# Performance work log

Hardware: AMD Instinct MI355X
Metric: run time of the kernel (lower is better)

The kernel has to match this reference:

```python
import jax, jax.numpy as jnp
import numpy as np

EPS = 1e-06


def setup_inputs() -> dict:
    key = jax.random.key(0)
    ks = jax.random.split(key, 6)
    B, H, S, W = 1, 12, 768, 32
    attn_logits = jax.random.normal(ks[0], (B, H, S, S), dtype=jnp.float32)
    # shared first linear: Linear(1, mlp_width) -> weight [W,1], bias [W]
    W_in = jax.random.normal(ks[1], (W, 1), dtype=jnp.float32) * (1.0)
    b_in = jax.random.normal(ks[2], (W,), dtype=jnp.float32) * 0.1
    # per-head output linear: Linear(mlp_width, 1) -> weight [H, W], bias [H]
    W_out = jax.random.normal(ks[3], (H, W), dtype=jnp.float32) / np.sqrt(W)
    b_out = jax.random.normal(ks[4], (H,), dtype=jnp.float32) * 0.1
    c = jnp.asarray(0.1, dtype=jnp.float32)
    L_multiplier = jnp.asarray(1.0, dtype=jnp.float32)
    init_L = jnp.asarray(512.0, dtype=jnp.float32)  # requires_grad=False in torch
    return {"attn_logits": attn_logits, "W_in": W_in, "b_in": b_in,
            "W_out": W_out, "b_out": b_out, "c": c,
            "L_multiplier": L_multiplier, "init_L": init_L}


def reference(attn_logits, W_in, b_in, W_out, b_out, c, L_multiplier, init_L):
    # gates and reverse cumulative sum along the key axis
    gates = jax.nn.sigmoid(attn_logits)                      # [B,H,S,S]
    pos = jax.lax.cumsum(gates, axis=3, reverse=True)        # flip-cumsum-flip
    numerator = jnp.log(jnp.abs(c * pos) + 1.0)
    max_pos = pos[..., 0:1]                                  # [B,H,S,1]
    threshold = jnp.abs(L_multiplier * init_L)
    denominator = jnp.log(jnp.abs(c * jnp.minimum(max_pos, threshold)) + 1.0) + EPS
    dist = numerator / denominator                           # [B,H,S,S]
    # shared Linear(1,W) + ReLU, then per-head Linear(W,1)
    w1 = W_in[:, 0]                                          # [W]
    hidden = jax.nn.relu(dist[..., None] * w1 + b_in)        # [B,H,S,S,W]
    fire_bias = jnp.einsum('bhijw,hw->bhij', hidden, W_out) + b_out[None, :, None, None]
    return fire_bias
```

## Files before the change

### kernel.cpp

```cpp
#include <hip/hip_runtime.h>

#define EPS_F 1e-6f
#define S_DIM 768
#define W_DIM 32

__global__ __launch_bounds__(256) void cope_fire_kernel(
    const float* __restrict__ attn,
    const float* __restrict__ W_in,
    const float* __restrict__ b_in,
    const float* __restrict__ W_out,
    const float* __restrict__ b_out,
    const float* __restrict__ c_p,
    const float* __restrict__ Lm_p,
    const float* __restrict__ iL_p,
    float* __restrict__ out)
{
    const int row = blockIdx.x;
    const int h   = row / S_DIM;
    const int t   = threadIdx.x;
    const int lane = t & 63;
    const int wave = t >> 6;

    __shared__ float s_w1[W_DIM], s_bin[W_DIM], s_wout[W_DIM];
    __shared__ float s_wsum[12];

    if (t < W_DIM) {
        s_w1[t]   = W_in[t];
        s_bin[t]  = b_in[t];
        s_wout[t] = W_out[h * W_DIM + t];
    }

    const float* rowp = attn + (size_t)row * S_DIM;
    const float c   = c_p[0];
    const float thr = fabsf(Lm_p[0] * iL_p[0]);
    const float bo  = b_out[h];

    float g[3];
#pragma unroll
    for (int s = 0; s < 3; s++) {
        float x = rowp[s * 256 + t];
        g[s] = 1.0f / (1.0f + expf(-x));
    }

    float incl[3];
#pragma unroll
    for (int s = 0; s < 3; s++) {
        float x = g[s];
#pragma unroll
        for (int d = 1; d < 64; d <<= 1) {
            float y = __shfl_up(x, d, 64);
            if (lane >= d) x += y;
        }
        if (lane == 63) s_wsum[s * 4 + wave] = x;
        incl[s] = x;
    }
    __syncthreads();

    float segtot[3];
#pragma unroll
    for (int s = 0; s < 3; s++) {
        float w0 = s_wsum[s * 4 + 0];
        float w1 = s_wsum[s * 4 + 1];
        float w2 = s_wsum[s * 4 + 2];
        float w3 = s_wsum[s * 4 + 3];
        float woff = 0.0f;
        if (wave > 0) woff += w0;
        if (wave > 1) woff += w1;
        if (wave > 2) woff += w2;
        incl[s] += woff;
        segtot[s] = w0 + w1 + w2 + w3;
    }
    const float off1  = segtot[0];
    const float off2  = segtot[0] + segtot[1];
    const float total = off2 + segtot[2];
    incl[1] += off1;
    incl[2] += off2;

    const float den = logf(fabsf(c * fminf(total, thr)) + 1.0f) + EPS_F;
    const float inv_den = 1.0f / den;

    float* outp = out + (size_t)row * S_DIM;
#pragma unroll
    for (int s = 0; s < 3; s++) {
        float pos  = total - incl[s] + g[s];
        float dist = logf(fabsf(c * pos) + 1.0f) * inv_den;
        float acc = bo;
#pragma unroll
        for (int w = 0; w < W_DIM; w++) {
            float hv = fmaxf(dist * s_w1[w] + s_bin[w], 0.0f);
            acc += hv * s_wout[w];
        }
        outp[s * 256 + t] = acc;
    }
}

extern "C" void kernel_launch(void* const* d_in, const int* in_sizes, int n_in,
                              void* d_out, int out_size, void* d_ws, size_t ws_size,
                              hipStream_t stream) {
    const float* attn  = (const float*)d_in[0];
    const float* W_in  = (const float*)d_in[1];
    const float* b_in  = (const float*)d_in[2];
    const float* W_out = (const float*)d_in[3];
    const float* b_out = (const float*)d_in[4];
    const float* c_p   = (const float*)d_in[5];
    const float* Lm_p  = (const float*)d_in[6];
    const float* iL_p  = (const float*)d_in[7];
    float* out = (float*)d_out;

    const int H = 12;
    const int rows = H * S_DIM;
    cope_fire_kernel<<<rows, 256, 0, stream>>>(
        attn, W_in, b_in, W_out, b_out, c_p, Lm_p, iL_p, out);
}
```

Baseline: 126.5 us.

## Replace per-element MLP with piecewise-linear lookup over sorted ReLU breakpoints

A setup kernel sorts the ReLU breakpoints -b/w of the shared first linear layer and precomputes per-head slope/intercept pairs for each of the 33 intervals. The main kernel then computes each output as one FMA after a binary search over the breakpoints, instead of a 32-wide hidden-layer loop. It also maps one row per wavefront with 12 contiguous elements per lane, float4 loads and stores, a single wave-level scan, and fast exp/log/rcp intrinsics. The cost is an extra tiny kernel launch and small float rounding differences from the reassociated arithmetic and fast math.

```diff
diff --git a/kernel.cpp b/kernel.cpp
--- a/kernel.cpp
+++ b/kernel.cpp
@@ -1,97 +1,135 @@
 #include <hip/hip_runtime.h>
+#include <math.h>
 
 #define EPS_F 1e-6f
 #define S_DIM 768
 #define W_DIM 32
+#define H_DIM 12
+#define NK 33
+
+
+__global__ __launch_bounds__(512) void cope_setup_kernel(
+    const float* __restrict__ W_in, const float* __restrict__ b_in,
+    const float* __restrict__ W_out, const float* __restrict__ b_out,
+    float* __restrict__ ws)
+{
+    __shared__ float th[W_DIM];
+    __shared__ int   rk[W_DIM];
+    const int t = threadIdx.x;
+
+    if (t < W_DIM) {
+        float w1 = W_in[t], b = b_in[t];
+        th[t] = (w1 != 0.0f) ? (-b / w1) : __builtin_inff();
+    }
+    __syncthreads();
+
+    if (t < W_DIM) {
+        float mine = th[t];
+        int r = 0;
+        for (int v = 0; v < W_DIM; v++) {
+            float o = th[v];
+            if (o < mine || (o == mine && v < t)) r++;
+        }
+        rk[t] = r;
+        ws[r] = mine;
+    }
+    __syncthreads();
+
+    if (t < H_DIM * NK) {
+        int h = t / NK, k = t % NK;
+        float A = 0.0f, B = b_out[h];
+        for (int w = 0; w < W_DIM; w++) {
+            float w1 = W_in[w], bv = b_in[w], ov = W_out[h * W_DIM + w];
+            bool active = (w1 > 0.0f) ? (k > rk[w])
+                        : (w1 < 0.0f) ? (k <= rk[w])
+                        : (bv > 0.0f);
+            if (active) { A += w1 * ov; B += bv * ov; }
+        }
+        ws[W_DIM + h * 2 * NK + 2 * k]     = A;
+        ws[W_DIM + h * 2 * NK + 2 * k + 1] = B;
+    }
+}
 
 __global__ __launch_bounds__(256) void cope_fire_kernel(
     const float* __restrict__ attn,
-    const float* __restrict__ W_in,
-    const float* __restrict__ b_in,
-    const float* __restrict__ W_out,
-    const float* __restrict__ b_out,
     const float* __restrict__ c_p,
     const float* __restrict__ Lm_p,
     const float* __restrict__ iL_p,
+    const float* __restrict__ ws,
     float* __restrict__ out)
 {
-    const int row = blockIdx.x;
-    const int h   = row / S_DIM;
-    const int t   = threadIdx.x;
+    const int t    = threadIdx.x;
     const int lane = t & 63;
     const int wave = t >> 6;
+    const int row  = blockIdx.x * 4 + wave;
+    const int h    = blockIdx.x / (S_DIM / 4);
 
-    __shared__ float s_w1[W_DIM], s_bin[W_DIM], s_wout[W_DIM];
-    __shared__ float s_wsum[12];
+    __shared__ float sh[W_DIM];
+    __shared__ float sAB[2 * NK];
 
-    if (t < W_DIM) {
-        s_w1[t]   = W_in[t];
-        s_bin[t]  = b_in[t];
-        s_wout[t] = W_out[h * W_DIM + t];
+    if (t < W_DIM)  sh[t]  = ws[t];
+    if (t < 2 * NK) sAB[t] = ws[W_DIM + h * 2 * NK + t];
+
+    const float s3 = ws[3],  s7 = ws[7],  s11 = ws[11], s15 = ws[15];
+    const float s19 = ws[19], s23 = ws[23], s27 = ws[27];
+    const float c   = c_p[0];
+    const float thr = fabsf(Lm_p[0] * iL_p[0]);
+
+    const float* rowp = attn + (size_t)row * S_DIM + lane * 12;
+    float4 v0 = *(const float4*)(rowp);
+    float4 v1 = *(const float4*)(rowp + 4);
+    float4 v2 = *(const float4*)(rowp + 8);
+    float g[12] = { v0.x, v0.y, v0.z, v0.w, v1.x, v1.y, v1.z, v1.w,
+                    v2.x, v2.y, v2.z, v2.w };
+#pragma unroll
+    for (int i = 0; i < 12; i++)
+        g[i] = __builtin_amdgcn_rcpf(1.0f + __expf(-g[i]));
+
+    float T0 = 0.0f;
+#pragma unroll
+    for (int i = 0; i < 12; i++) T0 += g[i];
+    float P = T0;
+#pragma unroll
+    for (int d = 1; d < 64; d <<= 1) {
+        float y = __shfl_up(P, d, 64);
+        if (lane >= d) P += y;
+    }
+    const float total = __shfl(P, 63, 64);
+    const float base  = total - P + T0;
+
+    const float den     = __logf(fabsf(c * fminf(total, thr)) + 1.0f) + EPS_F;
+    const float inv_den = __builtin_amdgcn_rcpf(den);
+
+    __syncthreads();
+
+    float o[12];
+    float e = 0.0f;
+#pragma unroll
+    for (int i = 0; i < 12; i++) {
+        float pos = base - e;
+        e += g[i];
+        float d = __logf(fabsf(c * pos) + 1.0f) * inv_den;
+
+        int k = 0;
+        bool b1 = (s15 < d);             if (b1) k += 16;
+        float l2 = b1 ? s23 : s7;
+        bool b2 = (l2 < d);              if (b2) k += 8;
+        float l3a = b2 ? s11 : s3;
+        float l3b = b2 ? s27 : s19;
+        float l3  = b1 ? l3b : l3a;
+        if (l3 < d) k += 4;
+        if (sh[k + 1] < d) k += 2;
+        if (sh[k]     < d) k += 1;
+        if (sh[k]     < d) k += 1;
+
+        float2 ab = *(const float2*)(&sAB[2 * k]);
+        o[i] = fmaf(d, ab.x, ab.y);
     }
 
-    const float* rowp = attn + (size_t)row * S_DIM;
-    const float c   = c_p[0];
-    const float thr = fabsf(Lm_p[0] * iL_p[0]);
-    const float bo  = b_out[h];
-
-    float g[3];
-#pragma unroll
-    for (int s = 0; s < 3; s++) {
-        float x = rowp[s * 256 + t];
-        g[s] = 1.0f / (1.0f + expf(-x));
-    }
-
-    float incl[3];
-#pragma unroll
-    for (int s = 0; s < 3; s++) {
-        float x = g[s];
-#pragma unroll
-        for (int d = 1; d < 64; d <<= 1) {
-            float y = __shfl_up(x, d, 64);
-            if (lane >= d) x += y;
-        }
-        if (lane == 63) s_wsum[s * 4 + wave] = x;
-        incl[s] = x;
-    }
-    __syncthreads();
-
-    float segtot[3];
-#pragma unroll
-    for (int s = 0; s < 3; s++) {
-        float w0 = s_wsum[s * 4 + 0];
-        float w1 = s_wsum[s * 4 + 1];
-        float w2 = s_wsum[s * 4 + 2];
-        float w3 = s_wsum[s * 4 + 3];
-        float woff = 0.0f;
-        if (wave > 0) woff += w0;
-        if (wave > 1) woff += w1;
-        if (wave > 2) woff += w2;
-        incl[s] += woff;
-        segtot[s] = w0 + w1 + w2 + w3;
-    }
-    const float off1  = segtot[0];
-    const float off2  = segtot[0] + segtot[1];
-    const float total = off2 + segtot[2];
-    incl[1] += off1;
-    incl[2] += off2;
-
-    const float den = logf(fabsf(c * fminf(total, thr)) + 1.0f) + EPS_F;
-    const float inv_den = 1.0f / den;
-
-    float* outp = out + (size_t)row * S_DIM;
-#pragma unroll
-    for (int s = 0; s < 3; s++) {
-        float pos  = total - incl[s] + g[s];
-        float dist = logf(fabsf(c * pos) + 1.0f) * inv_den;
-        float acc = bo;
-#pragma unroll
-        for (int w = 0; w < W_DIM; w++) {
-            float hv = fmaxf(dist * s_w1[w] + s_bin[w], 0.0f);
-            acc += hv * s_wout[w];
-        }
-        outp[s * 256 + t] = acc;
-    }
+    float* op = out + (size_t)row * S_DIM + lane * 12;
+    *(float4*)(op)     = make_float4(o[0], o[1], o[2],  o[3]);
+    *(float4*)(op + 4) = make_float4(o[4], o[5], o[6],  o[7]);
+    *(float4*)(op + 8) = make_float4(o[8], o[9], o[10], o[11]);
 }
 
 extern "C" void kernel_launch(void* const* d_in, const int* in_sizes, int n_in,
@@ -106,9 +144,11 @@
     const float* Lm_p  = (const float*)d_in[6];
     const float* iL_p  = (const float*)d_in[7];
     float* out = (float*)d_out;
+    float* ws  = (float*)d_ws;
 
-    const int H = 12;
-    const int rows = H * S_DIM;
-    cope_fire_kernel<<<rows, 256, 0, stream>>>(
-        attn, W_in, b_in, W_out, b_out, c_p, Lm_p, iL_p, out);
+    cope_setup_kernel<<<1, 512, 0, stream>>>(W_in, b_in, W_out, b_out, ws);
+
+    const int rows = H_DIM * S_DIM;
+    cope_fire_kernel<<<rows / 4, 256, 0, stream>>>(
+        attn, c_p, Lm_p, iL_p, ws, out);
 }
```

Result: faster. 102.8 us (-18.7%).
